# Optimization experiments

Hardware: AMD Instinct MI355X
Metric: run time of the kernel (lower is better)

Reference implementation:

```python
import jax, jax.numpy as jnp
import numpy as np

B, S, D, H = 4, 2048, 1024, 16
DK = D // H
NEG = -1.0e9

def setup_inputs() -> dict:
    key = jax.random.key(0)
    ks = jax.random.split(key, 9)
    scale = 1.0 / np.sqrt(D)
    x = jax.random.normal(ks[0], (B, S, D), dtype=jnp.float32)
    # causal mask: positions with mask==0 are filled with -1e9
    mask = jnp.tril(jnp.ones((S, S), dtype=jnp.int32))[None, None]  # [1,1,S,S]
    Wq = jax.random.normal(ks[1], (D, D), dtype=jnp.float32) * scale
    bq = jax.random.normal(ks[2], (D,), dtype=jnp.float32) * 0.01
    Wk = jax.random.normal(ks[3], (D, D), dtype=jnp.float32) * scale
    bk = jax.random.normal(ks[4], (D,), dtype=jnp.float32) * 0.01
    Wv = jax.random.normal(ks[5], (D, D), dtype=jnp.float32) * scale
    bv = jax.random.normal(ks[6], (D,), dtype=jnp.float32) * 0.01
    Wo = jax.random.normal(ks[7], (D, D), dtype=jnp.float32) * scale
    bo = jax.random.normal(ks[8], (D,), dtype=jnp.float32) * 0.01
    return {"x": x, "mask": mask, "Wq": Wq, "bq": bq, "Wk": Wk, "bk": bk,
            "Wv": Wv, "bv": bv, "Wo": Wo, "bo": bo}

def reference(x, mask, Wq, bq, Wk, bk, Wv, bv, Wo, bo):
    Bb, Ss, Dd = x.shape
    q = (x @ Wq.T + bq).reshape(Bb, Ss, H, DK).transpose(0, 2, 1, 3)  # [B,H,S,DK]
    k = (x @ Wk.T + bk).reshape(Bb, Ss, H, DK).transpose(0, 2, 1, 3)
    v = (x @ Wv.T + bv).reshape(Bb, Ss, H, DK).transpose(0, 2, 1, 3)
    scaled = jnp.einsum('bhqd,bhkd->bhqk', q, k) / jnp.sqrt(jnp.float32(DK))
    scaled = jnp.where(mask == 0, jnp.float32(NEG), scaled)
    attn = jax.nn.softmax(scaled, axis=-1)  # dropout prob = 0 -> identity
    vals = jnp.einsum('bhqk,bhkd->bhqd', attn, v)  # [B,H,S,DK]
    vals = vals.transpose(0, 2, 1, 3).reshape(Bb, Ss, H * DK)
    out = vals @ Wo.T + bo
    return out
```

## Files before the change

### kernel.cpp

```cpp
#include <hip/hip_runtime.h>
#include <hip/hip_bf16.h>
#include <cstdint>

#define B_ 4
#define S_ 2048
#define D_ 1024
#define H_ 16
#define DK_ 64

typedef _Float16 h8 __attribute__((ext_vector_type(8)));
typedef _Float16 h4 __attribute__((ext_vector_type(4)));
typedef float f32x4 __attribute__((ext_vector_type(4)));
typedef float f32x16 __attribute__((ext_vector_type(16)));
typedef unsigned int u32x4 __attribute__((ext_vector_type(4)));

__device__ __forceinline__ void gload16(const void* src, void* lds) {
  __builtin_amdgcn_global_load_lds((const __attribute__((address_space(1))) void*)src,
                                   (__attribute__((address_space(3))) void*)lds, 16, 0, 0);
}

__global__ __launch_bounds__(256) void conv_all(
    const float* __restrict__ x,
    const float* __restrict__ Wq, const float* __restrict__ Wk,
    const float* __restrict__ Wv, const float* __restrict__ Wo,
    const float* __restrict__ bq, const float* __restrict__ bk,
    const float* __restrict__ bv,
    _Float16* __restrict__ xb, _Float16* __restrict__ wqkv,
    _Float16* __restrict__ wo, float* __restrict__ bqkv) {
  const int bid = blockIdx.x, tid = threadIdx.x;
  if (bid < 4096) {
    int base = (bid * 256 + tid) * 8;
    h8 o;
#pragma unroll
    for (int j = 0; j < 8; ++j) o[j] = (_Float16)x[base + j];
    *(h8*)(xb + base) = o;
  } else {
    int i = (bid - 4096) * 256 + tid;
    int seg = i >> 17, r = i & 131071;
    const float* src = seg == 0 ? Wq : seg == 1 ? Wk : seg == 2 ? Wv : Wo;
    int base = r * 8;
    h8 o;
#pragma unroll
    for (int j = 0; j < 8; ++j) o[j] = (_Float16)src[base + j];
    if (seg < 3)
      *(h8*)(wqkv + (size_t)seg * 1048576 + base) = o;
    else
      *(h8*)(wo + base) = o;
    if (i < 768) {
      int bsel = i >> 8, k = (i & 255) * 4;
      const float* bs = bsel == 0 ? bq : bsel == 1 ? bk : bv;
      float4 v = *(const float4*)(bs + k);
      *(float4*)(bqkv + bsel * 1024 + k) = v;
    }
  }
}

template <int MODE>
__global__ __launch_bounds__(256) void gemm_nt(const _Float16* __restrict__ A,
                                               const _Float16* __restrict__ Bw,
                                               const float* __restrict__ bias,
                                               void* __restrict__ Cout,
                                               _Float16* __restrict__ Vt) {
  constexpr int K = D_;
  __shared__ unsigned short lds[2 * 128 * 64];
  char* ldsA = (char*)lds;
  char* ldsB = (char*)(lds + 128 * 64);

  const int tid = threadIdx.x;
  const int w = tid >> 6, lane = tid & 63, g = lane >> 4, c = lane & 15;
  const int wr = w >> 1, wc = w & 1;
  const int bn = blockIdx.x;
  const int bm = blockIdx.y;

  f32x4 acc[4][4] = {};

  const int srow = tid >> 3;
  const int scolsw = ((tid & 7) * 16) ^ ((srow & 7) << 4);
  const char* Ab = (const char*)(A + (size_t)bm * 128 * K);
  const char* Bb = (const char*)(Bw + (size_t)bn * 128 * K);
  const char* Asrc[4];
  const char* Bsrc[4];
#pragma unroll
  for (int j = 0; j < 4; ++j) {
    int row = j * 32 + srow;
    Asrc[j] = Ab + (size_t)row * (K * 2) + scolsw;
    Bsrc[j] = Bb + (size_t)row * (K * 2) + scolsw;
  }
  char* dstA = ldsA + w * 1024;
  char* dstB = ldsB + w * 1024;

  for (int k0 = 0; k0 < K; k0 += 64) {
    __syncthreads();
#pragma unroll
    for (int j = 0; j < 4; ++j) {
      gload16(Asrc[j] + k0 * 2, dstA + j * 4096);
      gload16(Bsrc[j] + k0 * 2, dstB + j * 4096);
    }
    __syncthreads();
#pragma unroll
    for (int kk = 0; kk < 2; ++kk) {
      h8 a[4], b[4];
#pragma unroll
      for (int mi = 0; mi < 4; ++mi) {
        int row = wr * 64 + mi * 16 + c;
        int off = row * 128 + kk * 64 + g * 16;
        a[mi] = *(const h8*)(ldsA + (off ^ ((row & 7) << 4)));
      }
#pragma unroll
      for (int ni = 0; ni < 4; ++ni) {
        int row = wc * 64 + ni * 16 + c;
        int off = row * 128 + kk * 64 + g * 16;
        b[ni] = *(const h8*)(ldsB + (off ^ ((row & 7) << 4)));
      }
      __builtin_amdgcn_s_setprio(1);
#pragma unroll
      for (int mi = 0; mi < 4; ++mi)
#pragma unroll
        for (int ni = 0; ni < 4; ++ni)
          acc[mi][ni] = __builtin_amdgcn_mfma_f32_16x16x32_f16(a[mi], b[ni], acc[mi][ni], 0, 0, 0);
      __builtin_amdgcn_s_setprio(0);
    }
  }

  if (MODE == 0 && bn >= 16) {
#pragma unroll
    for (int mi = 0; mi < 4; ++mi)
#pragma unroll
      for (int ni = 0; ni < 4; ++ni) {
        int m0 = bm * 128 + wr * 64 + mi * 16 + g * 4;
        int n = bn * 128 + wc * 64 + ni * 16 + c;
        float bb = bias[n];
        h4 v4;
#pragma unroll
        for (int r = 0; r < 4; ++r) v4[r] = (_Float16)(acc[mi][ni][r] + bb);
        int bI = m0 >> 11, sI = m0 & 2047;
        int dk = n & 63, hh = (n >> 6) & 15;
        *(h4*)(Vt + (((size_t)(bI * 16 + hh) * 64 + dk) * 2048 + sI)) = v4;
      }
  } else {
#pragma unroll
    for (int mi = 0; mi < 4; ++mi)
#pragma unroll
      for (int ni = 0; ni < 4; ++ni)
#pragma unroll
        for (int r = 0; r < 4; ++r) {
          int m = bm * 128 + wr * 64 + mi * 16 + g * 4 + r;
          int n = bn * 128 + wc * 64 + ni * 16 + c;
          float v = acc[mi][ni][r] + bias[n];
          if (MODE == 0) {
            int which = n >> 10, nn = n & 1023;
            int bI = m >> 11, sI = m & 2047, hI = nn >> 6, dkI = nn & 63;
            ((_Float16*)Cout)[(size_t)which * 8388608 +
                              (((size_t)bI * H_ + hI) * S_ + sI) * DK_ + dkI] = (_Float16)v;
          } else {
            ((float*)Cout)[(size_t)m * D_ + n] = v;
          }
        }
  }
}

__global__ __launch_bounds__(512) void attn_fwd(const _Float16* __restrict__ Q,
                                                const _Float16* __restrict__ K,
                                                const _Float16* __restrict__ Vt,
                                                _Float16* __restrict__ vals) {
  __shared__ char lds[2 * 16384];

  const int tid = threadIdx.x;
  const int w = tid >> 6;
  const int lane = tid & 63;
  const int l31 = lane & 31, hi = lane >> 5;
  const int bid = blockIdx.x;
  const int pi = bid >> 6;
  const int bh = bid & 63;
  const int bI = bh >> 4, hI = bh & 15;

  const char* Qb = (const char*)(Q + (size_t)bh * S_ * DK_);
  const char* Kb = (const char*)(K + (size_t)bh * S_ * DK_);
  const char* Vtb = (const char*)(Vt + (size_t)bh * DK_ * S_);

  const int srow = tid >> 3;
  const int colsw = ((tid & 7) * 16) ^ ((srow & 7) << 4);
  const int offK = srow * 128 + colsw;
  const int offV = srow * 4096 + colsw;

  int rdo[4];
#pragma unroll
  for (int ks = 0; ks < 4; ++ks)
    rdo[ks] = l31 * 128 + ((ks * 32 + hi * 16) ^ ((l31 & 7) << 4));

  auto stage = [&](char* buf, int kv0) {
    gload16(Kb + (size_t)kv0 * 128 + offK, buf + w * 1024);
    gload16(Vtb + (size_t)kv0 * 2 + offV, buf + 8192 + w * 1024);
  };

  const _Float16 qsc = (_Float16)(0.125f * 1.44269504f);

  for (int phase = 0; phase < 2; ++phase) {
    const int sup = (phase == 0) ? pi : 7 - pi;
    const int qw = sup * 8 + w;
    const int nt = 4 * sup + 4;

    h8 qf[4];
#pragma unroll
    for (int ks = 0; ks < 4; ++ks) {
      h8 v = *(const h8*)(Qb + (size_t)(qw * 32 + l31) * 128 + ks * 32 + hi * 16);
#pragma unroll
      for (int j = 0; j < 8; ++j) v[j] *= qsc;
      qf[ks] = v;
    }

    f32x16 o[2] = {};
    float m_ = -1e30f, l_ = 0.f;

    stage(lds, 0);
    __syncthreads();

    for (int t = 0; t < nt; ++t) {
      const int cur = t & 1;
      const char* ldsb = lds + cur * 16384;
      if (t + 1 < nt) stage(lds + (cur ^ 1) * 16384, (t + 1) * 64);

      const int rel = qw - 2 * t;
      if (rel >= 0) {
        const bool have1 = (rel >= 1);

        f32x16 s0 = {}, s1 = {};
#pragma unroll
        for (int ks = 0; ks < 4; ++ks) {
          h8 k0 = *(const h8*)(ldsb + rdo[ks]);
          __builtin_amdgcn_s_setprio(1);
          s0 = __builtin_amdgcn_mfma_f32_32x32x16_f16(k0, qf[ks], s0, 0, 0, 0);
          __builtin_amdgcn_s_setprio(0);
          if (have1) {
            h8 k1 = *(const h8*)(ldsb + 4096 + rdo[ks]);
            __builtin_amdgcn_s_setprio(1);
            s1 = __builtin_amdgcn_mfma_f32_32x32x16_f16(k1, qf[ks], s1, 0, 0, 0);
            __builtin_amdgcn_s_setprio(0);
          }
        }

        if (rel == 0) {
#pragma unroll
          for (int r = 0; r < 16; ++r) {
            int rowidx = (r & 3) + 8 * (r >> 2) + 4 * hi;
            if (rowidx > l31) s0[r] = -1e30f;
          }
        } else if (rel == 1) {
#pragma unroll
          for (int r = 0; r < 16; ++r) {
            int rowidx = (r & 3) + 8 * (r >> 2) + 4 * hi;
            if (rowidx > l31) s1[r] = -1e30f;
          }
        }

        float t8[8];
#pragma unroll
        for (int j = 0; j < 8; ++j) t8[j] = fmaxf(s0[2 * j], s0[2 * j + 1]);
        if (have1)
#pragma unroll
          for (int j = 0; j < 8; ++j) t8[j] = fmaxf(t8[j], fmaxf(s1[2 * j], s1[2 * j + 1]));
        float t4a = fmaxf(t8[0], t8[1]), t4b = fmaxf(t8[2], t8[3]);
        float t4c = fmaxf(t8[4], t8[5]), t4d = fmaxf(t8[6], t8[7]);
        float pmax = fmaxf(fmaxf(t4a, t4b), fmaxf(t4c, t4d));

        if (!__all(pmax <= m_ + 8.f)) {
          float rm = fmaxf(pmax, __shfl_xor(pmax, 32));
          float mn = fmaxf(m_, rm);
          float al = __builtin_amdgcn_exp2f(m_ - mn);
          m_ = mn;
          l_ *= al;
#pragma unroll
          for (int r = 0; r < 16; ++r) {
            float av = __shfl(al, (r & 3) + 8 * (r >> 2) + 4 * hi);
            o[0][r] *= av;
            o[1][r] *= av;
          }
        }

        unsigned int u0[8], u1[8];
        float rsa = 0.f, rsb = 0.f;
#pragma unroll
        for (int j = 0; j < 8; ++j) {
          float e0 = __builtin_amdgcn_exp2f(s0[2 * j] - m_);
          float e1 = __builtin_amdgcn_exp2f(s0[2 * j + 1] - m_);
          rsa += e0 + e1;
          u0[j] = __builtin_bit_cast(unsigned int, __builtin_amdgcn_cvt_pkrtz(e0, e1));
        }
        if (have1) {
#pragma unroll
          for (int j = 0; j < 8; ++j) {
            float e0 = __builtin_amdgcn_exp2f(s1[2 * j] - m_);
            float e1 = __builtin_amdgcn_exp2f(s1[2 * j + 1] - m_);
            rsb += e0 + e1;
            u1[j] = __builtin_bit_cast(unsigned int, __builtin_amdgcn_cvt_pkrtz(e0, e1));
          }
        }
        l_ += rsa + rsb;

        h8 pa0[2], pa1[2];
#pragma unroll
        for (int b = 0; b < 2; ++b) {
          unsigned int ua = u0[4 * b], ub = u0[4 * b + 1];
          unsigned int uc = u0[4 * b + 2], ud = u0[4 * b + 3];
          unsigned int va = hi ? ua : uc, vb = hi ? ub : ud;
          unsigned int xa = __shfl_xor(va, 32), xb = __shfl_xor(vb, 32);
          u32x4 q = {hi ? xa : ua, hi ? xb : ub, hi ? uc : xa, hi ? ud : xb};
          pa0[b] = __builtin_bit_cast(h8, q);
        }
        if (have1) {
#pragma unroll
          for (int b = 0; b < 2; ++b) {
            unsigned int ua = u1[4 * b], ub = u1[4 * b + 1];
            unsigned int uc = u1[4 * b + 2], ud = u1[4 * b + 3];
            unsigned int va = hi ? ua : uc, vb = hi ? ub : ud;
            unsigned int xa = __shfl_xor(va, 32), xb = __shfl_xor(vb, 32);
            u32x4 q = {hi ? xa : ua, hi ? xb : ub, hi ? uc : xa, hi ? ud : xb};
            pa1[b] = __builtin_bit_cast(h8, q);
          }
        }

#pragma unroll
        for (int x = 0; x < 2; ++x) {
#pragma unroll
          for (int kvs = 0; kvs < 4; ++kvs) {
            int ni = kvs >> 1, b = kvs & 1;
            if (!have1 && ni == 1) continue;
            h8 vf = *(const h8*)(ldsb + 8192 + x * 4096 + rdo[kvs]);
            h8 pa = ni ? pa1[b] : pa0[b];
            __builtin_amdgcn_s_setprio(1);
            o[x] = __builtin_amdgcn_mfma_f32_32x32x16_f16(pa, vf, o[x], 0, 0, 0);
            __builtin_amdgcn_s_setprio(0);
          }
        }
      }

      __syncthreads();
    }

    float lt = l_ + __shfl_xor(l_, 32);
    float linv = 1.0f / lt;
#pragma unroll
    for (int r = 0; r < 16; ++r) {
      int qidx = (r & 3) + 8 * (r >> 2) + 4 * hi;
      float inv = __shfl(linv, qidx);
      int qrow = qw * 32 + qidx;
      size_t rowoff = ((size_t)bI * S_ + qrow) * D_ + hI * 64 + l31;
      vals[rowoff] = (_Float16)(o[0][r] * inv);
      vals[rowoff + 32] = (_Float16)(o[1][r] * inv);
    }
  }
}

extern "C" void kernel_launch(void* const* d_in, const int* in_sizes, int n_in,
                              void* d_out, int out_size, void* d_ws, size_t ws_size,
                              hipStream_t stream) {
  const float* x  = (const float*)d_in[0];
  const float* Wq = (const float*)d_in[2];
  const float* bq = (const float*)d_in[3];
  const float* Wk = (const float*)d_in[4];
  const float* bk = (const float*)d_in[5];
  const float* Wv = (const float*)d_in[6];
  const float* bv = (const float*)d_in[7];
  const float* Wo = (const float*)d_in[8];
  const float* bo = (const float*)d_in[9];
  float* out = (float*)d_out;

  char* ws = (char*)d_ws;
  size_t off = 0;
  auto alloc = [&](size_t bytes) {
    char* p = ws + off;
    off += (bytes + 255) & ~(size_t)255;
    return p;
  };
  _Float16* xb   = (_Float16*)alloc((size_t)B_ * S_ * D_ * 2);
  _Float16* wqkv = (_Float16*)alloc((size_t)3 * D_ * D_ * 2);
  _Float16* wob  = (_Float16*)alloc((size_t)D_ * D_ * 2);
  float*    bqkv = (float*)alloc((size_t)3 * D_ * 4);
  _Float16* qkvw = (_Float16*)alloc((size_t)2 * B_ * H_ * S_ * DK_ * 2);
  _Float16* Vtw  = (_Float16*)alloc((size_t)B_ * H_ * S_ * DK_ * 2);
  _Float16* valw = (_Float16*)alloc((size_t)B_ * S_ * D_ * 2);

  conv_all<<<6144, 256, 0, stream>>>(x, Wq, Wk, Wv, Wo, bq, bk, bv, xb, wqkv, wob, bqkv);

  gemm_nt<0><<<dim3(24, 64), 256, 0, stream>>>(xb, wqkv, bqkv, qkvw, Vtw);

  attn_fwd<<<256, 512, 0, stream>>>(qkvw, qkvw + (size_t)8388608, Vtw, valw);

  gemm_nt<1><<<dim3(8, 64), 256, 0, stream>>>(valw, wob, bo, out, nullptr);
}
```

Baseline: 176.9 us.

## Deepen LDS pipelines in GEMM and attention with fine-grained vmcnt waits

The projection GEMM moves to 256x128 tiles with 512 threads and a 5-slot LDS ring that keeps three K-steps of global-to-LDS loads in flight. It waits with explicit vmcnt counts and a single barrier per step, replacing the two __syncthreads per step. The attention kernel goes from double to triple buffering of K/V tiles with the same counted-wait scheme, and both kernels switch to a k-chunk-major LDS layout with no XOR swizzle. The aim is to hide global load latency and cut barrier stalls, at the cost of more LDS per block and possible LDS bank conflicts from the unswizzled reads.

```diff
diff --git a/kernel.cpp b/kernel.cpp
--- a/kernel.cpp
+++ b/kernel.cpp
@@ -56,79 +56,77 @@
 }
 
 template <int MODE>
-__global__ __launch_bounds__(256) void gemm_nt(const _Float16* __restrict__ A,
+__global__ __launch_bounds__(512) void gemm_nt(const _Float16* __restrict__ A,
                                                const _Float16* __restrict__ Bw,
                                                const float* __restrict__ bias,
                                                void* __restrict__ Cout,
                                                _Float16* __restrict__ Vt) {
-  constexpr int K = D_;
-  __shared__ unsigned short lds[2 * 128 * 64];
-  char* ldsA = (char*)lds;
-  char* ldsB = (char*)(lds + 128 * 64);
+  __shared__ char lds[5 * 24576];
 
   const int tid = threadIdx.x;
   const int w = tid >> 6, lane = tid & 63, g = lane >> 4, c = lane & 15;
-  const int wr = w >> 1, wc = w & 1;
+  const int wm = w >> 1, wn = w & 1;
   const int bn = blockIdx.x;
   const int bm = blockIdx.y;
 
+  const char* Ab = (const char*)(A + (size_t)bm * 256 * D_);
+  const char* Bb = (const char*)(Bw + (size_t)bn * 128 * D_);
+
+  const size_t arow = (size_t)((w & 3) * 64 + lane) * 2048;
+  const int akb = (w >> 2) * 16;
+  const size_t brow = (size_t)((w & 1) * 64 + lane) * 2048;
+  const int bkb = (w >> 1) * 16;
+  auto stageU = [&](int v) {
+    char* slot = lds + (v % 5) * 24576;
+    const size_t kbyte = (size_t)v * 64;
+    gload16(Ab + arow + kbyte + akb, slot + w * 1024);
+    gload16(Ab + arow + kbyte + akb + 32, slot + 8192 + w * 1024);
+    gload16(Bb + brow + kbyte + bkb, slot + 16384 + w * 1024);
+  };
+
   f32x4 acc[4][4] = {};
 
-  const int srow = tid >> 3;
-  const int scolsw = ((tid & 7) * 16) ^ ((srow & 7) << 4);
-  const char* Ab = (const char*)(A + (size_t)bm * 128 * K);
-  const char* Bb = (const char*)(Bw + (size_t)bn * 128 * K);
-  const char* Asrc[4];
-  const char* Bsrc[4];
-#pragma unroll
-  for (int j = 0; j < 4; ++j) {
-    int row = j * 32 + srow;
-    Asrc[j] = Ab + (size_t)row * (K * 2) + scolsw;
-    Bsrc[j] = Bb + (size_t)row * (K * 2) + scolsw;
+  stageU(0); stageU(1); stageU(2);
+  asm volatile("s_waitcnt vmcnt(6)" ::: "memory");
+  __builtin_amdgcn_s_barrier();
+  asm volatile("" ::: "memory");
+
+  for (int u = 0; u < 32; ++u) {
+    if (u + 3 < 32) stageU(u + 3);
+    const char* slot = lds + (u % 5) * 24576;
+
+    h8 a[4], b[4];
+#pragma unroll
+    for (int mi = 0; mi < 4; ++mi)
+      a[mi] = *(const h8*)(slot + g * 4096 + ((wm * 64 + mi * 16 + c) << 4));
+#pragma unroll
+    for (int ni = 0; ni < 4; ++ni)
+      b[ni] = *(const h8*)(slot + 16384 + g * 2048 + ((wn * 64 + ni * 16 + c) << 4));
+    __builtin_amdgcn_s_setprio(1);
+#pragma unroll
+    for (int mi = 0; mi < 4; ++mi)
+#pragma unroll
+      for (int ni = 0; ni < 4; ++ni)
+        acc[mi][ni] = __builtin_amdgcn_mfma_f32_16x16x32_f16(a[mi], b[ni], acc[mi][ni], 0, 0, 0);
+    __builtin_amdgcn_s_setprio(0);
+
+    if (u < 29)
+      asm volatile("s_waitcnt vmcnt(6)" ::: "memory");
+    else if (u == 29)
+      asm volatile("s_waitcnt vmcnt(3)" ::: "memory");
+    else
+      asm volatile("s_waitcnt vmcnt(0)" ::: "memory");
+    __builtin_amdgcn_s_barrier();
+    asm volatile("" ::: "memory");
   }
-  char* dstA = ldsA + w * 1024;
-  char* dstB = ldsB + w * 1024;
-
-  for (int k0 = 0; k0 < K; k0 += 64) {
-    __syncthreads();
-#pragma unroll
-    for (int j = 0; j < 4; ++j) {
-      gload16(Asrc[j] + k0 * 2, dstA + j * 4096);
-      gload16(Bsrc[j] + k0 * 2, dstB + j * 4096);
-    }
-    __syncthreads();
-#pragma unroll
-    for (int kk = 0; kk < 2; ++kk) {
-      h8 a[4], b[4];
-#pragma unroll
-      for (int mi = 0; mi < 4; ++mi) {
-        int row = wr * 64 + mi * 16 + c;
-        int off = row * 128 + kk * 64 + g * 16;
-        a[mi] = *(const h8*)(ldsA + (off ^ ((row & 7) << 4)));
-      }
+
+  if (MODE == 0 && bn >= 16) {
+#pragma unroll
+    for (int mi = 0; mi < 4; ++mi)
 #pragma unroll
       for (int ni = 0; ni < 4; ++ni) {
-        int row = wc * 64 + ni * 16 + c;
-        int off = row * 128 + kk * 64 + g * 16;
-        b[ni] = *(const h8*)(ldsB + (off ^ ((row & 7) << 4)));
-      }
-      __builtin_amdgcn_s_setprio(1);
-#pragma unroll
-      for (int mi = 0; mi < 4; ++mi)
-#pragma unroll
-        for (int ni = 0; ni < 4; ++ni)
-          acc[mi][ni] = __builtin_amdgcn_mfma_f32_16x16x32_f16(a[mi], b[ni], acc[mi][ni], 0, 0, 0);
-      __builtin_amdgcn_s_setprio(0);
-    }
-  }
-
-  if (MODE == 0 && bn >= 16) {
-#pragma unroll
-    for (int mi = 0; mi < 4; ++mi)
-#pragma unroll
-      for (int ni = 0; ni < 4; ++ni) {
-        int m0 = bm * 128 + wr * 64 + mi * 16 + g * 4;
-        int n = bn * 128 + wc * 64 + ni * 16 + c;
+        int m0 = bm * 256 + wm * 64 + mi * 16 + g * 4;
+        int n = bn * 128 + wn * 64 + ni * 16 + c;
         float bb = bias[n];
         h4 v4;
 #pragma unroll
@@ -144,8 +142,8 @@
       for (int ni = 0; ni < 4; ++ni)
 #pragma unroll
         for (int r = 0; r < 4; ++r) {
-          int m = bm * 128 + wr * 64 + mi * 16 + g * 4 + r;
-          int n = bn * 128 + wc * 64 + ni * 16 + c;
+          int m = bm * 256 + wm * 64 + mi * 16 + g * 4 + r;
+          int n = bn * 128 + wn * 64 + ni * 16 + c;
           float v = acc[mi][ni][r] + bias[n];
           if (MODE == 0) {
             int which = n >> 10, nn = n & 1023;
@@ -163,7 +161,7 @@
                                                 const _Float16* __restrict__ K,
                                                 const _Float16* __restrict__ Vt,
                                                 _Float16* __restrict__ vals) {
-  __shared__ char lds[2 * 16384];
+  __shared__ char lds[3 * 16384];
 
   const int tid = threadIdx.x;
   const int w = tid >> 6;
@@ -178,20 +176,15 @@
   const char* Kb = (const char*)(K + (size_t)bh * S_ * DK_);
   const char* Vtb = (const char*)(Vt + (size_t)bh * DK_ * S_);
 
-  const int srow = tid >> 3;
-  const int colsw = ((tid & 7) * 16) ^ ((srow & 7) << 4);
-  const int offK = srow * 128 + colsw;
-  const int offV = srow * 4096 + colsw;
+  auto stage = [&](int sloti, int kv0) {
+    char* buf = lds + sloti * 16384;
+    gload16(Kb + (size_t)kv0 * 128 + (size_t)lane * 128 + w * 16, buf + w * 1024);
+    gload16(Vtb + (size_t)lane * 4096 + (size_t)kv0 * 2 + w * 16, buf + 8192 + w * 1024);
+  };
 
   int rdo[4];
 #pragma unroll
-  for (int ks = 0; ks < 4; ++ks)
-    rdo[ks] = l31 * 128 + ((ks * 32 + hi * 16) ^ ((l31 & 7) << 4));
-
-  auto stage = [&](char* buf, int kv0) {
-    gload16(Kb + (size_t)kv0 * 128 + offK, buf + w * 1024);
-    gload16(Vtb + (size_t)kv0 * 2 + offV, buf + 8192 + w * 1024);
-  };
+  for (int ks = 0; ks < 4; ++ks) rdo[ks] = (ks * 2 + hi) * 1024 + l31 * 16;
 
   const _Float16 qsc = (_Float16)(0.125f * 1.44269504f);
 
@@ -212,13 +205,15 @@
     f32x16 o[2] = {};
     float m_ = -1e30f, l_ = 0.f;
 
-    stage(lds, 0);
-    __syncthreads();
+    stage(0, 0);
+    stage(1, 64);
+    asm volatile("s_waitcnt vmcnt(2)" ::: "memory");
+    __builtin_amdgcn_s_barrier();
+    asm volatile("" ::: "memory");
 
     for (int t = 0; t < nt; ++t) {
-      const int cur = t & 1;
-      const char* ldsb = lds + cur * 16384;
-      if (t + 1 < nt) stage(lds + (cur ^ 1) * 16384, (t + 1) * 64);
+      const char* ldsb = lds + (t % 3) * 16384;
+      if (t + 2 < nt) stage((t + 2) % 3, (t + 2) * 64);
 
       const int rel = qw - 2 * t;
       if (rel >= 0) {
@@ -232,7 +227,7 @@
           s0 = __builtin_amdgcn_mfma_f32_32x32x16_f16(k0, qf[ks], s0, 0, 0, 0);
           __builtin_amdgcn_s_setprio(0);
           if (have1) {
-            h8 k1 = *(const h8*)(ldsb + 4096 + rdo[ks]);
+            h8 k1 = *(const h8*)(ldsb + rdo[ks] + 512);
             __builtin_amdgcn_s_setprio(1);
             s1 = __builtin_amdgcn_mfma_f32_32x32x16_f16(k1, qf[ks], s1, 0, 0, 0);
             __builtin_amdgcn_s_setprio(0);
@@ -325,7 +320,7 @@
           for (int kvs = 0; kvs < 4; ++kvs) {
             int ni = kvs >> 1, b = kvs & 1;
             if (!have1 && ni == 1) continue;
-            h8 vf = *(const h8*)(ldsb + 8192 + x * 4096 + rdo[kvs]);
+            h8 vf = *(const h8*)(ldsb + 8192 + rdo[kvs] + x * 512);
             h8 pa = ni ? pa1[b] : pa0[b];
             __builtin_amdgcn_s_setprio(1);
             o[x] = __builtin_amdgcn_mfma_f32_32x32x16_f16(pa, vf, o[x], 0, 0, 0);
@@ -334,7 +329,12 @@
         }
       }
 
-      __syncthreads();
+      if (t + 2 < nt)
+        asm volatile("s_waitcnt vmcnt(2)" ::: "memory");
+      else
+        asm volatile("s_waitcnt vmcnt(0)" ::: "memory");
+      __builtin_amdgcn_s_barrier();
+      asm volatile("" ::: "memory");
     }
 
     float lt = l_ + __shfl_xor(l_, 32);
@@ -382,9 +382,9 @@
 
   conv_all<<<6144, 256, 0, stream>>>(x, Wq, Wk, Wv, Wo, bq, bk, bv, xb, wqkv, wob, bqkv);
 
-  gemm_nt<0><<<dim3(24, 64), 256, 0, stream>>>(xb, wqkv, bqkv, qkvw, Vtw);
+  gemm_nt<0><<<dim3(24, 32), 512, 0, stream>>>(xb, wqkv, bqkv, qkvw, Vtw);
 
   attn_fwd<<<256, 512, 0, stream>>>(qkvw, qkvw + (size_t)8388608, Vtw, valw);
 
-  gemm_nt<1><<<dim3(8, 64), 256, 0, stream>>>(valw, wob, bo, out, nullptr);
-}
+  gemm_nt<1><<<dim3(8, 32), 512, 0, stream>>>(valw, wob, bo, out, nullptr);
+}
```

Measured after the change: 237.7 us. +34.4%, slower.

## Use 256x128 tiles for QKV GEMM and triple-buffer attention K/V loads

Applied to the files above, without the earlier changes.

The QKV projection moves into a dedicated kernel with 256x128 output tiles, a K-major LDS layout filled straight from global memory, and a 128-wide K step, which raises reuse per LDS load and halves the number of M blocks. The attention kernel switches from double to triple buffering of K/V tiles, using explicit vmcnt waits and raw barriers so two tiles are in flight at once, and drops the XOR swizzle in favour of a K-chunk-major LDS layout. This costs more LDS and registers per block, the larger tile may lower occupancy, and removing the swizzle could add LDS bank conflicts.

```diff
diff --git a/kernel.cpp b/kernel.cpp
--- a/kernel.cpp
+++ b/kernel.cpp
@@ -55,12 +55,93 @@
   }
 }
 
-template <int MODE>
-__global__ __launch_bounds__(256) void gemm_nt(const _Float16* __restrict__ A,
-                                               const _Float16* __restrict__ Bw,
-                                               const float* __restrict__ bias,
-                                               void* __restrict__ Cout,
-                                               _Float16* __restrict__ Vt) {
+__global__ __launch_bounds__(256, 2) void gemm_qkv(const _Float16* __restrict__ A,
+                                                   const _Float16* __restrict__ Bw,
+                                                   const float* __restrict__ bias,
+                                                   _Float16* __restrict__ QKout,
+                                                   _Float16* __restrict__ Vt) {
+  __shared__ char lds[49152];
+
+  const int tid = threadIdx.x;
+  const int w = tid >> 6, lane = tid & 63, g = lane >> 4, c = lane & 15;
+  const int wm = w >> 1, wn = w & 1;
+  const int bn = blockIdx.x;
+  const int bm = blockIdx.y;
+
+  const char* Ab = (const char*)A + (size_t)(bm * 256 + tid) * 2048;
+  const char* Bb = (const char*)Bw + (size_t)(bn * 128 + (tid & 127)) * 2048;
+  const int bkb16 = (tid >> 7) * 16;
+
+  f32x4 acc[8][4] = {};
+
+  for (int k0 = 0; k0 < 2048; k0 += 128) {
+    __syncthreads();
+#pragma unroll
+    for (int j = 0; j < 8; ++j)
+      gload16(Ab + k0 + j * 16, lds + j * 4096 + w * 1024);
+#pragma unroll
+    for (int j = 0; j < 4; ++j)
+      gload16(Bb + k0 + j * 32 + bkb16, lds + 32768 + j * 4096 + w * 1024);
+    __syncthreads();
+
+#pragma unroll
+    for (int kk = 0; kk < 2; ++kk) {
+      h8 b[4];
+#pragma unroll
+      for (int ni = 0; ni < 4; ++ni)
+        b[ni] = *(const h8*)(lds + 32768 +
+                             (((kk * 4 + g) * 128 + wn * 64 + ni * 16 + c) << 4));
+      h8 a[8];
+#pragma unroll
+      for (int mi = 0; mi < 8; ++mi)
+        a[mi] = *(const h8*)(lds + (((kk * 4 + g) * 256 + wm * 128 + mi * 16 + c) << 4));
+      __builtin_amdgcn_s_setprio(1);
+#pragma unroll
+      for (int mi = 0; mi < 8; ++mi)
+#pragma unroll
+        for (int ni = 0; ni < 4; ++ni)
+          acc[mi][ni] = __builtin_amdgcn_mfma_f32_16x16x32_f16(a[mi], b[ni], acc[mi][ni], 0, 0, 0);
+      __builtin_amdgcn_s_setprio(0);
+    }
+  }
+
+  if (bn >= 16) {
+#pragma unroll
+    for (int mi = 0; mi < 8; ++mi)
+#pragma unroll
+      for (int ni = 0; ni < 4; ++ni) {
+        int m0 = bm * 256 + wm * 128 + mi * 16 + g * 4;
+        int n = bn * 128 + wn * 64 + ni * 16 + c;
+        float bb = bias[n];
+        h4 v4;
+#pragma unroll
+        for (int r = 0; r < 4; ++r) v4[r] = (_Float16)(acc[mi][ni][r] + bb);
+        int bI = m0 >> 11, sI = m0 & 2047;
+        int dk = n & 63, hh = (n >> 6) & 15;
+        *(h4*)(Vt + (((size_t)(bI * 16 + hh) * 64 + dk) * 2048 + sI)) = v4;
+      }
+  } else {
+#pragma unroll
+    for (int mi = 0; mi < 8; ++mi)
+#pragma unroll
+      for (int ni = 0; ni < 4; ++ni)
+#pragma unroll
+        for (int r = 0; r < 4; ++r) {
+          int m = bm * 256 + wm * 128 + mi * 16 + g * 4 + r;
+          int n = bn * 128 + wn * 64 + ni * 16 + c;
+          float v = acc[mi][ni][r] + bias[n];
+          int which = n >> 10, nn = n & 1023;
+          int bI = m >> 11, sI = m & 2047, hI = nn >> 6, dkI = nn & 63;
+          QKout[(size_t)which * 8388608 +
+                (((size_t)bI * H_ + hI) * S_ + sI) * DK_ + dkI] = (_Float16)v;
+        }
+  }
+}
+
+__global__ __launch_bounds__(256) void gemm_out(const _Float16* __restrict__ A,
+                                                const _Float16* __restrict__ Bw,
+                                                const float* __restrict__ bias,
+                                                float* __restrict__ Cout) {
   constexpr int K = D_;
   __shared__ unsigned short lds[2 * 128 * 64];
   char* ldsA = (char*)lds;
@@ -122,48 +203,23 @@
     }
   }
 
-  if (MODE == 0 && bn >= 16) {
-#pragma unroll
-    for (int mi = 0; mi < 4; ++mi)
-#pragma unroll
-      for (int ni = 0; ni < 4; ++ni) {
-        int m0 = bm * 128 + wr * 64 + mi * 16 + g * 4;
+#pragma unroll
+  for (int mi = 0; mi < 4; ++mi)
+#pragma unroll
+    for (int ni = 0; ni < 4; ++ni)
+#pragma unroll
+      for (int r = 0; r < 4; ++r) {
+        int m = bm * 128 + wr * 64 + mi * 16 + g * 4 + r;
         int n = bn * 128 + wc * 64 + ni * 16 + c;
-        float bb = bias[n];
-        h4 v4;
-#pragma unroll
-        for (int r = 0; r < 4; ++r) v4[r] = (_Float16)(acc[mi][ni][r] + bb);
-        int bI = m0 >> 11, sI = m0 & 2047;
-        int dk = n & 63, hh = (n >> 6) & 15;
-        *(h4*)(Vt + (((size_t)(bI * 16 + hh) * 64 + dk) * 2048 + sI)) = v4;
+        Cout[(size_t)m * D_ + n] = acc[mi][ni][r] + bias[n];
       }
-  } else {
-#pragma unroll
-    for (int mi = 0; mi < 4; ++mi)
-#pragma unroll
-      for (int ni = 0; ni < 4; ++ni)
-#pragma unroll
-        for (int r = 0; r < 4; ++r) {
-          int m = bm * 128 + wr * 64 + mi * 16 + g * 4 + r;
-          int n = bn * 128 + wc * 64 + ni * 16 + c;
-          float v = acc[mi][ni][r] + bias[n];
-          if (MODE == 0) {
-            int which = n >> 10, nn = n & 1023;
-            int bI = m >> 11, sI = m & 2047, hI = nn >> 6, dkI = nn & 63;
-            ((_Float16*)Cout)[(size_t)which * 8388608 +
-                              (((size_t)bI * H_ + hI) * S_ + sI) * DK_ + dkI] = (_Float16)v;
-          } else {
-            ((float*)Cout)[(size_t)m * D_ + n] = v;
-          }
-        }
-  }
 }
 
 __global__ __launch_bounds__(512) void attn_fwd(const _Float16* __restrict__ Q,
                                                 const _Float16* __restrict__ K,
                                                 const _Float16* __restrict__ Vt,
                                                 _Float16* __restrict__ vals) {
-  __shared__ char lds[2 * 16384];
+  __shared__ char lds[3 * 16384];
 
   const int tid = threadIdx.x;
   const int w = tid >> 6;
@@ -178,20 +234,15 @@
   const char* Kb = (const char*)(K + (size_t)bh * S_ * DK_);
   const char* Vtb = (const char*)(Vt + (size_t)bh * DK_ * S_);
 
-  const int srow = tid >> 3;
-  const int colsw = ((tid & 7) * 16) ^ ((srow & 7) << 4);
-  const int offK = srow * 128 + colsw;
-  const int offV = srow * 4096 + colsw;
+  auto stage = [&](int sloti, int kv0) {
+    char* buf = lds + sloti * 16384;
+    gload16(Kb + (size_t)kv0 * 128 + (size_t)lane * 128 + w * 16, buf + w * 1024);
+    gload16(Vtb + (size_t)lane * 4096 + (size_t)kv0 * 2 + w * 16, buf + 8192 + w * 1024);
+  };
 
   int rdo[4];
 #pragma unroll
-  for (int ks = 0; ks < 4; ++ks)
-    rdo[ks] = l31 * 128 + ((ks * 32 + hi * 16) ^ ((l31 & 7) << 4));
-
-  auto stage = [&](char* buf, int kv0) {
-    gload16(Kb + (size_t)kv0 * 128 + offK, buf + w * 1024);
-    gload16(Vtb + (size_t)kv0 * 2 + offV, buf + 8192 + w * 1024);
-  };
+  for (int ks = 0; ks < 4; ++ks) rdo[ks] = (ks * 2 + hi) * 1024 + l31 * 16;
 
   const _Float16 qsc = (_Float16)(0.125f * 1.44269504f);
 
@@ -212,13 +263,15 @@
     f32x16 o[2] = {};
     float m_ = -1e30f, l_ = 0.f;
 
-    stage(lds, 0);
-    __syncthreads();
+    stage(0, 0);
+    stage(1, 64);
+    asm volatile("s_waitcnt vmcnt(2)" ::: "memory");
+    __builtin_amdgcn_s_barrier();
+    asm volatile("" ::: "memory");
 
     for (int t = 0; t < nt; ++t) {
-      const int cur = t & 1;
-      const char* ldsb = lds + cur * 16384;
-      if (t + 1 < nt) stage(lds + (cur ^ 1) * 16384, (t + 1) * 64);
+      const char* ldsb = lds + (t % 3) * 16384;
+      if (t + 2 < nt) stage((t + 2) % 3, (t + 2) * 64);
 
       const int rel = qw - 2 * t;
       if (rel >= 0) {
@@ -232,7 +285,7 @@
           s0 = __builtin_amdgcn_mfma_f32_32x32x16_f16(k0, qf[ks], s0, 0, 0, 0);
           __builtin_amdgcn_s_setprio(0);
           if (have1) {
-            h8 k1 = *(const h8*)(ldsb + 4096 + rdo[ks]);
+            h8 k1 = *(const h8*)(ldsb + rdo[ks] + 512);
             __builtin_amdgcn_s_setprio(1);
             s1 = __builtin_amdgcn_mfma_f32_32x32x16_f16(k1, qf[ks], s1, 0, 0, 0);
             __builtin_amdgcn_s_setprio(0);
@@ -325,7 +378,7 @@
           for (int kvs = 0; kvs < 4; ++kvs) {
             int ni = kvs >> 1, b = kvs & 1;
             if (!have1 && ni == 1) continue;
-            h8 vf = *(const h8*)(ldsb + 8192 + x * 4096 + rdo[kvs]);
+            h8 vf = *(const h8*)(ldsb + 8192 + rdo[kvs] + x * 512);
             h8 pa = ni ? pa1[b] : pa0[b];
             __builtin_amdgcn_s_setprio(1);
             o[x] = __builtin_amdgcn_mfma_f32_32x32x16_f16(pa, vf, o[x], 0, 0, 0);
@@ -334,7 +387,12 @@
         }
       }
 
-      __syncthreads();
+      if (t + 2 < nt)
+        asm volatile("s_waitcnt vmcnt(2)" ::: "memory");
+      else
+        asm volatile("s_waitcnt vmcnt(0)" ::: "memory");
+      __builtin_amdgcn_s_barrier();
+      asm volatile("" ::: "memory");
     }
 
     float lt = l_ + __shfl_xor(l_, 32);
@@ -382,9 +440,9 @@
 
   conv_all<<<6144, 256, 0, stream>>>(x, Wq, Wk, Wv, Wo, bq, bk, bv, xb, wqkv, wob, bqkv);
 
-  gemm_nt<0><<<dim3(24, 64), 256, 0, stream>>>(xb, wqkv, bqkv, qkvw, Vtw);
+  gemm_qkv<<<dim3(24, 32), 256, 0, stream>>>(xb, wqkv, bqkv, qkvw, Vtw);
 
   attn_fwd<<<256, 512, 0, stream>>>(qkvw, qkvw + (size_t)8388608, Vtw, valw);
 
-  gemm_nt<1><<<dim3(8, 64), 256, 0, stream>>>(valw, wob, bo, out, nullptr);
-}
+  gemm_out<<<dim3(8, 64), 256, 0, stream>>>(valw, wob, bo, out);
+}
```

New measurement: 219.1 us. 1.24x slower.
